# Kernel tuning notes

Measured on AMD Instinct MI355X. Metric: run time of the kernel, lower is better.

## Reference

```python
import jax, jax.numpy as jnp
import numpy as np

ALPHA1 = 0.1
ALPHA2 = 0.1
NOISE = 0.02
B, T, H, O = 128, 512, 512, 3


def setup_inputs() -> dict:
    key = jax.random.key(0)
    ks = jax.random.split(key, 10)
    return {
        "x": jax.random.normal(ks[0], (B, T, 5), dtype=jnp.float32),
        "wi_stim": jax.random.normal(ks[1], (3, H), dtype=jnp.float32) / np.sqrt(3),
        "wrec11": jax.random.normal(ks[2], (H, H), dtype=jnp.float32) / np.sqrt(H),
        "wi_ctx": jax.random.normal(ks[3], (2, H), dtype=jnp.float32) / np.sqrt(2),
        "wrec22": jax.random.normal(ks[4], (H, H), dtype=jnp.float32) / np.sqrt(H),
        "wrec12": jax.random.normal(ks[5], (H, H), dtype=jnp.float32) / np.sqrt(H),
        "wrec21": jax.random.normal(ks[6], (H, H), dtype=jnp.float32) / np.sqrt(H),
        "wo": jax.random.normal(ks[7], (H, O), dtype=jnp.float32) / np.sqrt(H),
        "noise1": jax.random.normal(ks[8], (T, B, H), dtype=jnp.float32),
        "noise2": jax.random.normal(ks[9], (T, B, H), dtype=jnp.float32),
    }


def reference(x, wi_stim, wrec11, wi_ctx, wrec22, wrec12, wrec21, wo, noise1, noise2):
    # x: [B, T, 5]; noise: [T, B, H] (pre-sampled standard normals, scaled by NOISE)
    xs = jnp.transpose(x[:, :, :3], (1, 0, 2))  # [T, B, 3]
    xc = jnp.transpose(x[:, :, 3:], (1, 0, 2))  # [T, B, 2]

    def step(carry, inp):
        h1, h2 = carry
        xsi, xci, n1, n2 = inp
        h1 = (1 - ALPHA1) * h1 + ALPHA1 * (
            xsi @ wi_stim + jnp.tanh(h1) @ wrec11 + jnp.tanh(h2) @ wrec12 + n1 * NOISE
        )
        # note: h2 update uses the freshly-updated h1 (as in the torch loop)
        h2 = (1 - ALPHA2) * h2 + ALPHA2 * (
            xci @ wi_ctx + jnp.tanh(h1) @ wrec21 + jnp.tanh(h2) @ wrec22 + n2 * NOISE
        )
        return (h1, h2), jnp.tanh(h2) @ wo

    h0 = jnp.zeros((x.shape[0], wrec11.shape[0]), dtype=x.dtype)
    _, out_t = jax.lax.scan(step, (h0, h0), (xs, xc, noise1, noise2))  # [T, B, O]
    return jnp.transpose(out_t, (1, 0, 2))  # [B, T, O]
```

## Files before the change

### kernel.cpp

```cpp
#include <hip/hip_runtime.h>
#include <hip/hip_bf16.h>

#define TT 512
#define BB 128
#define HH 512
#define NGROUP 8
#define NSLICE 8
#define ALPHA 0.1f
#define NOISE_S 0.02f

typedef __attribute__((ext_vector_type(8))) short short8;
typedef __attribute__((ext_vector_type(8))) _Float16 half8;
typedef __attribute__((ext_vector_type(4))) float f32x4;

#define WPACK_CH 132096
#define PUB1_B (WPACK_CH * 16)
#define PUB2_B (PUB1_B + NGROUP * 16384)
#define FLAG_B (PUB2_B + NGROUP * 16384)

__device__ __forceinline__ unsigned short f2h(float f) {
  return __builtin_bit_cast(unsigned short, (_Float16)f);
}

__device__ __forceinline__ float fast_tanh(float x) {
  float e = __builtin_amdgcn_exp2f(x * 2.8853900817779268f);
  return 1.0f - 2.0f * __builtin_amdgcn_rcpf(e + 1.0f);
}

__device__ __forceinline__ f32x4 mfma16(short8 a, short8 b, f32x4 c) {
  return __builtin_amdgcn_mfma_f32_16x16x32_f16(
      __builtin_bit_cast(half8, a), __builtin_bit_cast(half8, b), c, 0, 0, 0);
}

__global__ void pack_weights(const float* __restrict__ w11, const float* __restrict__ w12,
                             const float* __restrict__ w21, const float* __restrict__ w22,
                             const float* __restrict__ wo, unsigned short* __restrict__ dst) {
  int idx = blockIdx.x * 256 + threadIdx.x;
  if (idx < 131072) {
    int which = idx >> 16;
    int c0 = idx & 65535;
    int kt = c0 >> 11, rem = c0 & 2047;
    int nt = rem >> 6, lane = rem & 63;
    const float* wlo = which ? w21 : w11;
    const float* whi = which ? w22 : w12;
    unsigned short* p = dst + (size_t)idx * 8;
    int n = nt * 16 + (lane & 15);
    int kb = kt * 32 + ((lane >> 4) & 3) * 8;
#pragma unroll
    for (int i = 0; i < 8; ++i) {
      int k = kb + i;
      float v = (k < HH) ? wlo[k * HH + n] : whi[(k - HH) * HH + n];
      p[i] = f2h(v);
    }
  } else if (idx < 132096) {
    int c0 = idx - 131072;
    int kt = c0 >> 6, lane = c0 & 63;
    unsigned short* p = dst + (size_t)131072 * 8 + (size_t)c0 * 8;
    int n = lane & 15;
    int kb = kt * 32 + ((lane >> 4) & 3) * 8;
#pragma unroll
    for (int i = 0; i < 8; ++i) {
      float v = (n < 3) ? wo[(kb + i) * 3 + n] : 0.0f;
      p[i] = f2h(v);
    }
  }
}

__global__ void zero_flags(int* __restrict__ f) {
  f[blockIdx.x * 1024 + threadIdx.x] = 0;
}

__global__ __launch_bounds__(256, 1)
void rnn_main(const float* __restrict__ x, const float* __restrict__ wi_stim,
              const float* __restrict__ wi_ctx, const float* __restrict__ noise1,
              const float* __restrict__ noise2, char* __restrict__ ws,
              float* __restrict__ out) {
  __shared__ __align__(16) unsigned short T1buf[16 * 512];
  __shared__ __align__(16) unsigned short T2buf[16 * 512];
  __shared__ __align__(16) unsigned short WOlds[16 * 512];
  __shared__ float xstage[2][16][5];

  const int tid = threadIdx.x;
  const int w = tid >> 6, lane = tid & 63;
  const int c16 = lane & 15, kh = lane >> 4;
  const int g = blockIdx.x & (NGROUP - 1);
  const int slice = blockIdx.x >> 3;
  const int nt = slice * 4 + w;
  const int n0 = nt * 16;
  const int b0 = g * 16;
  const int lrow0 = kh * 4;

  const short8* __restrict__ WC = (const short8*)ws;
  unsigned short* __restrict__ pub1 = (unsigned short*)(ws + PUB1_B) + g * 8192;
  unsigned short* __restrict__ pub2 = (unsigned short*)(ws + PUB2_B) + g * 8192;
  int* __restrict__ flags = (int*)(ws + FLAG_B) + g * (2 * TT);

  short8 z = {0, 0, 0, 0, 0, 0, 0, 0};
  for (int i = tid; i < 1024; i += 256) {
    ((short8*)T1buf)[i] = z;
    ((short8*)T2buf)[i] = z;
  }
  if (slice == 0) {
#pragma unroll
    for (int c = 0; c < 4; ++c) {
      int kt = w * 4 + c;
      short8 v = WC[131072 + kt * 64 + lane];
      *(short8*)&WOlds[kt * 512 + lane * 8] = v;
    }
  }
  if (tid < 80) {
    int b = tid / 5, c = tid % 5;
    xstage[0][b][c] = x[((size_t)(b0 + b) * TT + 0) * 5 + c];
  }

  float wis[3], wic[2];
#pragma unroll
  for (int c = 0; c < 3; ++c) wis[c] = wi_stim[c * HH + n0 + c16];
#pragma unroll
  for (int c = 0; c < 2; ++c) wic[c] = wi_ctx[c * HH + n0 + c16];

  float h1[4] = {0, 0, 0, 0}, h2[4] = {0, 0, 0, 0};

  const int kt_p = nt >> 1;
  const int hi = (((nt & 1) * 16) + c16) >> 3;
  const int ci = c16 & 7;

  const short8* __restrict__ WAp = WC + nt * 64 + lane;
  const short8* __restrict__ WBp = WC + 65536 + nt * 64 + lane;

  __syncthreads();

  for (int t = 0; t < TT; ++t) {
    const int buf = t & 1;

    float n1v[4], n2v[4];
#pragma unroll
    for (int r = 0; r < 4; ++r) {
      size_t rowoff = ((size_t)t * BB + b0 + lrow0 + r) * HH + n0 + c16;
      n1v[r] = noise1[rowoff];
      n2v[r] = noise2[rowoff];
    }

    f32x4 aA = {0, 0, 0, 0}, aB = {0, 0, 0, 0};
#pragma unroll
    for (int kt = 0; kt < 16; ++kt) {
      short8 a1 = *(const short8*)&T1buf[kt * 512 + lane * 8];
      aA = mfma16(a1, WAp[kt * 2048], aA);
      short8 a2 = *(const short8*)&T2buf[kt * 512 + lane * 8];
      aB = mfma16(a2, WAp[(16 + kt) * 2048], aB);
    }
    unsigned short tp[4];
#pragma unroll
    for (int r = 0; r < 4; ++r) {
      float pre = aA[r] + aB[r]
                + wis[0] * xstage[buf][lrow0 + r][0]
                + wis[1] * xstage[buf][lrow0 + r][1]
                + wis[2] * xstage[buf][lrow0 + r][2]
                + NOISE_S * n1v[r];
      float h = (1.0f - ALPHA) * h1[r] + ALPHA * pre;
      h1[r] = h;
      tp[r] = f2h(fast_tanh(h));
    }
#pragma unroll
    for (int r = 0; r < 4; ++r)
      __hip_atomic_store(&pub1[kt_p * 512 + (lrow0 + r + hi * 16) * 8 + ci], tp[r],
                         __ATOMIC_RELAXED, __HIP_MEMORY_SCOPE_AGENT);
    asm volatile("s_waitcnt vmcnt(0)" ::: "memory");
    __syncthreads();
    if (tid == 0)
      __hip_atomic_fetch_add(&flags[2 * t], 1, __ATOMIC_RELAXED,
                             __HIP_MEMORY_SCOPE_AGENT);

    f32x4 bA = {0, 0, 0, 0}, bB = {0, 0, 0, 0};
#pragma unroll
    for (int kt = 0; kt < 16; ++kt) {
      short8 a2 = *(const short8*)&T2buf[kt * 512 + lane * 8];
      bB = mfma16(a2, WBp[(16 + kt) * 2048], bB);
    }
    while (__hip_atomic_load(&flags[2 * t], __ATOMIC_RELAXED,
                             __HIP_MEMORY_SCOPE_AGENT) < NSLICE)
      __builtin_amdgcn_s_sleep(1);
    __builtin_amdgcn_sched_barrier(0);
    asm volatile("" ::: "memory");
#pragma unroll
    for (int c = 0; c < 4; ++c) {
      int kt = w * 4 + c;
      const unsigned long long* src =
          (const unsigned long long*)&pub1[kt * 512 + lane * 8];
      unsigned long long v0 = __hip_atomic_load(&src[0], __ATOMIC_RELAXED,
                                                __HIP_MEMORY_SCOPE_AGENT);
      unsigned long long v1 = __hip_atomic_load(&src[1], __ATOMIC_RELAXED,
                                                __HIP_MEMORY_SCOPE_AGENT);
      *(unsigned long long*)&T1buf[kt * 512 + lane * 8] = v0;
      *(unsigned long long*)&T1buf[kt * 512 + lane * 8 + 4] = v1;
    }
    __syncthreads();
#pragma unroll
    for (int kt = 0; kt < 16; ++kt) {
      short8 a1 = *(const short8*)&T1buf[kt * 512 + lane * 8];
      bA = mfma16(a1, WBp[kt * 2048], bA);
    }
#pragma unroll
    for (int r = 0; r < 4; ++r) {
      float pre = bA[r] + bB[r]
                + wic[0] * xstage[buf][lrow0 + r][3]
                + wic[1] * xstage[buf][lrow0 + r][4]
                + NOISE_S * n2v[r];
      float h = (1.0f - ALPHA) * h2[r] + ALPHA * pre;
      h2[r] = h;
      tp[r] = f2h(fast_tanh(h));
    }
#pragma unroll
    for (int r = 0; r < 4; ++r)
      __hip_atomic_store(&pub2[kt_p * 512 + (lrow0 + r + hi * 16) * 8 + ci], tp[r],
                         __ATOMIC_RELAXED, __HIP_MEMORY_SCOPE_AGENT);
    asm volatile("s_waitcnt vmcnt(0)" ::: "memory");
    __syncthreads();
    if (tid == 0)
      __hip_atomic_fetch_add(&flags[2 * t + 1], 1, __ATOMIC_RELAXED,
                             __HIP_MEMORY_SCOPE_AGENT);
    while (__hip_atomic_load(&flags[2 * t + 1], __ATOMIC_RELAXED,
                             __HIP_MEMORY_SCOPE_AGENT) < NSLICE)
      __builtin_amdgcn_s_sleep(1);
    __builtin_amdgcn_sched_barrier(0);
    asm volatile("" ::: "memory");
#pragma unroll
    for (int c = 0; c < 4; ++c) {
      int kt = w * 4 + c;
      const unsigned long long* src =
          (const unsigned long long*)&pub2[kt * 512 + lane * 8];
      unsigned long long v0 = __hip_atomic_load(&src[0], __ATOMIC_RELAXED,
                                                __HIP_MEMORY_SCOPE_AGENT);
      unsigned long long v1 = __hip_atomic_load(&src[1], __ATOMIC_RELAXED,
                                                __HIP_MEMORY_SCOPE_AGENT);
      *(unsigned long long*)&T2buf[kt * 512 + lane * 8] = v0;
      *(unsigned long long*)&T2buf[kt * 512 + lane * 8 + 4] = v1;
    }
    if (t + 1 < TT && tid < 80) {
      int b = tid / 5, c = tid % 5;
      xstage[buf ^ 1][b][c] = x[((size_t)(b0 + b) * TT + (t + 1)) * 5 + c];
    }
    __syncthreads();

    if (slice == 0 && w == 0) {
      f32x4 ao = {0, 0, 0, 0};
#pragma unroll
      for (int kt = 0; kt < 16; ++kt) {
        short8 a2 = *(const short8*)&T2buf[kt * 512 + lane * 8];
        short8 bo = *(const short8*)&WOlds[kt * 512 + lane * 8];
        ao = mfma16(a2, bo, ao);
      }
      if (c16 < 3) {
#pragma unroll
        for (int r = 0; r < 4; ++r)
          out[((size_t)(b0 + lrow0 + r) * TT + t) * 3 + c16] = ao[r];
      }
    }
  }
}

extern "C" void kernel_launch(void* const* d_in, const int* in_sizes, int n_in,
                              void* d_out, int out_size, void* d_ws, size_t ws_size,
                              hipStream_t stream) {
  const float* x       = (const float*)d_in[0];
  const float* wi_stim = (const float*)d_in[1];
  const float* w11     = (const float*)d_in[2];
  const float* wi_ctx  = (const float*)d_in[3];
  const float* w22     = (const float*)d_in[4];
  const float* w12     = (const float*)d_in[5];
  const float* w21     = (const float*)d_in[6];
  const float* wo      = (const float*)d_in[7];
  const float* n1      = (const float*)d_in[8];
  const float* n2      = (const float*)d_in[9];
  char* ws = (char*)d_ws;

  zero_flags<<<NGROUP, 1024, 0, stream>>>((int*)(ws + FLAG_B));
  pack_weights<<<516, 256, 0, stream>>>(w11, w12, w21, w22, wo,
                                        (unsigned short*)ws);
  rnn_main<<<NSLICE * NGROUP, 256, 0, stream>>>(x, wi_stim, wi_ctx, n1, n2, ws,
                                                (float*)d_out);
}
```

Baseline: 4.468 ms.

## Replace per-step atomic counters with per-slice flags and defer h2 gather

Swaps the per-timestep fetch_add counters for per-slice monotonic flags that a whole wave polls with a vote, without sleeping. The gather of the previous step's h2 moves to the start of the next step, after the h1 recurrence MFMAs, so one barrier per step drops out of the critical path. The output projection rotates across slices and is delayed by one step. Publication buffers are now zeroed so the first gather reads zeros. The cost is more polling traffic on flag cache lines and a more delicate ordering protocol.

```diff
diff --git a/kernel.cpp b/kernel.cpp
--- a/kernel.cpp
+++ b/kernel.cpp
@@ -66,8 +66,9 @@
   }
 }
 
-__global__ void zero_flags(int* __restrict__ f) {
-  f[blockIdx.x * 1024 + threadIdx.x] = 0;
+__global__ void zero_ws(int* __restrict__ p, int n) {
+  for (int i = blockIdx.x * 256 + threadIdx.x; i < n; i += gridDim.x * 256)
+    p[i] = 0;
 }
 
 __global__ __launch_bounds__(256, 1)
@@ -93,20 +94,19 @@
   const short8* __restrict__ WC = (const short8*)ws;
   unsigned short* __restrict__ pub1 = (unsigned short*)(ws + PUB1_B) + g * 8192;
   unsigned short* __restrict__ pub2 = (unsigned short*)(ws + PUB2_B) + g * 8192;
-  int* __restrict__ flags = (int*)(ws + FLAG_B) + g * (2 * TT);
+  int* __restrict__ fl1 = (int*)(ws + FLAG_B) + g * 8;
+  int* __restrict__ fl2 = (int*)(ws + FLAG_B) + NGROUP * 8 + g * 8;
 
   short8 z = {0, 0, 0, 0, 0, 0, 0, 0};
   for (int i = tid; i < 1024; i += 256) {
     ((short8*)T1buf)[i] = z;
     ((short8*)T2buf)[i] = z;
   }
-  if (slice == 0) {
-#pragma unroll
-    for (int c = 0; c < 4; ++c) {
-      int kt = w * 4 + c;
-      short8 v = WC[131072 + kt * 64 + lane];
-      *(short8*)&WOlds[kt * 512 + lane * 8] = v;
-    }
+#pragma unroll
+  for (int c = 0; c < 4; ++c) {
+    int kt = w * 4 + c;
+    short8 v = WC[131072 + kt * 64 + lane];
+    *(short8*)&WOlds[kt * 512 + lane * 8] = v;
   }
   if (tid < 80) {
     int b = tid / 5, c = tid % 5;
@@ -128,27 +128,68 @@
   const short8* __restrict__ WAp = WC + nt * 64 + lane;
   const short8* __restrict__ WBp = WC + 65536 + nt * 64 + lane;
 
+  auto poll = [&](int* f, int target) {
+    int v;
+    do {
+      v = (lane < 8) ? __hip_atomic_load(&f[lane], __ATOMIC_RELAXED,
+                                         __HIP_MEMORY_SCOPE_AGENT)
+                     : target;
+    } while (!__all(v >= target));
+    __builtin_amdgcn_sched_barrier(0);
+    asm volatile("" ::: "memory");
+  };
+
   __syncthreads();
 
   for (int t = 0; t < TT; ++t) {
     const int buf = t & 1;
 
-    float n1v[4], n2v[4];
-#pragma unroll
-    for (int r = 0; r < 4; ++r) {
-      size_t rowoff = ((size_t)t * BB + b0 + lrow0 + r) * HH + n0 + c16;
-      n1v[r] = noise1[rowoff];
-      n2v[r] = noise2[rowoff];
-    }
+    float n1v[4];
+#pragma unroll
+    for (int r = 0; r < 4; ++r)
+      n1v[r] = noise1[((size_t)t * BB + b0 + lrow0 + r) * HH + n0 + c16];
 
     f32x4 aA = {0, 0, 0, 0}, aB = {0, 0, 0, 0};
 #pragma unroll
     for (int kt = 0; kt < 16; ++kt) {
       short8 a1 = *(const short8*)&T1buf[kt * 512 + lane * 8];
       aA = mfma16(a1, WAp[kt * 2048], aA);
+    }
+    poll(fl2, t);
+#pragma unroll
+    for (int c = 0; c < 4; ++c) {
+      int kt = w * 4 + c;
+      const unsigned long long* src =
+          (const unsigned long long*)&pub2[kt * 512 + lane * 8];
+      unsigned long long v0 = __hip_atomic_load(&src[0], __ATOMIC_RELAXED,
+                                                __HIP_MEMORY_SCOPE_AGENT);
+      unsigned long long v1 = __hip_atomic_load(&src[1], __ATOMIC_RELAXED,
+                                                __HIP_MEMORY_SCOPE_AGENT);
+      *(unsigned long long*)&T2buf[kt * 512 + lane * 8] = v0;
+      *(unsigned long long*)&T2buf[kt * 512 + lane * 8 + 4] = v1;
+    }
+    __syncthreads();
+#pragma unroll
+    for (int kt = 0; kt < 16; ++kt) {
       short8 a2 = *(const short8*)&T2buf[kt * 512 + lane * 8];
       aB = mfma16(a2, WAp[(16 + kt) * 2048], aB);
     }
+
+    if (t > 0 && slice == ((t - 1) & 7) && w == 0) {
+      f32x4 ao = {0, 0, 0, 0};
+#pragma unroll
+      for (int kt = 0; kt < 16; ++kt) {
+        short8 a2 = *(const short8*)&T2buf[kt * 512 + lane * 8];
+        short8 bo = *(const short8*)&WOlds[kt * 512 + lane * 8];
+        ao = mfma16(a2, bo, ao);
+      }
+      if (c16 < 3) {
+#pragma unroll
+        for (int r = 0; r < 4; ++r)
+          out[((size_t)(b0 + lrow0 + r) * TT + (t - 1)) * 3 + c16] = ao[r];
+      }
+    }
+
     unsigned short tp[4];
 #pragma unroll
     for (int r = 0; r < 4; ++r) {
@@ -168,8 +209,13 @@
     asm volatile("s_waitcnt vmcnt(0)" ::: "memory");
     __syncthreads();
     if (tid == 0)
-      __hip_atomic_fetch_add(&flags[2 * t], 1, __ATOMIC_RELAXED,
-                             __HIP_MEMORY_SCOPE_AGENT);
+      __hip_atomic_store(&fl1[slice], t + 1, __ATOMIC_RELAXED,
+                         __HIP_MEMORY_SCOPE_AGENT);
+
+    float n2v[4];
+#pragma unroll
+    for (int r = 0; r < 4; ++r)
+      n2v[r] = noise2[((size_t)t * BB + b0 + lrow0 + r) * HH + n0 + c16];
 
     f32x4 bA = {0, 0, 0, 0}, bB = {0, 0, 0, 0};
 #pragma unroll
@@ -177,11 +223,7 @@
       short8 a2 = *(const short8*)&T2buf[kt * 512 + lane * 8];
       bB = mfma16(a2, WBp[(16 + kt) * 2048], bB);
     }
-    while (__hip_atomic_load(&flags[2 * t], __ATOMIC_RELAXED,
-                             __HIP_MEMORY_SCOPE_AGENT) < NSLICE)
-      __builtin_amdgcn_s_sleep(1);
-    __builtin_amdgcn_sched_barrier(0);
-    asm volatile("" ::: "memory");
+    poll(fl1, t + 1);
 #pragma unroll
     for (int c = 0; c < 4; ++c) {
       int kt = w * 4 + c;
@@ -193,6 +235,10 @@
                                                 __HIP_MEMORY_SCOPE_AGENT);
       *(unsigned long long*)&T1buf[kt * 512 + lane * 8] = v0;
       *(unsigned long long*)&T1buf[kt * 512 + lane * 8 + 4] = v1;
+    }
+    if (t + 1 < TT && tid < 80) {
+      int b = tid / 5, c = tid % 5;
+      xstage[buf ^ 1][b][c] = x[((size_t)(b0 + b) * TT + (t + 1)) * 5 + c];
     }
     __syncthreads();
 #pragma unroll
@@ -217,13 +263,12 @@
     asm volatile("s_waitcnt vmcnt(0)" ::: "memory");
     __syncthreads();
     if (tid == 0)
-      __hip_atomic_fetch_add(&flags[2 * t + 1], 1, __ATOMIC_RELAXED,
-                             __HIP_MEMORY_SCOPE_AGENT);
-    while (__hip_atomic_load(&flags[2 * t + 1], __ATOMIC_RELAXED,
-                             __HIP_MEMORY_SCOPE_AGENT) < NSLICE)
-      __builtin_amdgcn_s_sleep(1);
-    __builtin_amdgcn_sched_barrier(0);
-    asm volatile("" ::: "memory");
+      __hip_atomic_store(&fl2[slice], t + 1, __ATOMIC_RELAXED,
+                         __HIP_MEMORY_SCOPE_AGENT);
+  }
+
+  if (slice == ((TT - 1) & 7)) {
+    poll(fl2, TT);
 #pragma unroll
     for (int c = 0; c < 4; ++c) {
       int kt = w * 4 + c;
@@ -236,13 +281,8 @@
       *(unsigned long long*)&T2buf[kt * 512 + lane * 8] = v0;
       *(unsigned long long*)&T2buf[kt * 512 + lane * 8 + 4] = v1;
     }
-    if (t + 1 < TT && tid < 80) {
-      int b = tid / 5, c = tid % 5;
-      xstage[buf ^ 1][b][c] = x[((size_t)(b0 + b) * TT + (t + 1)) * 5 + c];
-    }
-    __syncthreads();
-
-    if (slice == 0 && w == 0) {
+    __syncthreads();
+    if (w == 0) {
       f32x4 ao = {0, 0, 0, 0};
 #pragma unroll
       for (int kt = 0; kt < 16; ++kt) {
@@ -253,7 +293,7 @@
       if (c16 < 3) {
 #pragma unroll
         for (int r = 0; r < 4; ++r)
-          out[((size_t)(b0 + lrow0 + r) * TT + t) * 3 + c16] = ao[r];
+          out[((size_t)(b0 + lrow0 + r) * TT + (TT - 1)) * 3 + c16] = ao[r];
       }
     }
   }
@@ -274,7 +314,8 @@
   const float* n2      = (const float*)d_in[9];
   char* ws = (char*)d_ws;
 
-  zero_flags<<<NGROUP, 1024, 0, stream>>>((int*)(ws + FLAG_B));
+  int nz = (NGROUP * 16384 * 2 + 2 * NGROUP * 8 * 4) / 4;
+  zero_ws<<<64, 256, 0, stream>>>((int*)(ws + PUB1_B), nz);
   pack_weights<<<516, 256, 0, stream>>>(w11, w12, w21, w22, wo,
                                         (unsigned short*)ws);
   rnn_main<<<NSLICE * NGROUP, 256, 0, stream>>>(x, wi_stim, wi_ctx, n1, n2, ws,
```

Result: faster. 3.745 ms (-16.2%).
